# Performance work log

Measured on AMD Instinct MI355X. Metric: run time of the kernel, lower is better.

Reference implementation:

```python
import jax, jax.numpy as jnp
import numpy as np

G = 1.0      # gravitational constant from G_Nbody(graph, 1.0, eps=1e-10)
EPS = 1e-10  # softening epsilon
N_BODIES = 4096


def setup_inputs() -> dict:
    key = jax.random.key(0)
    kx, = jax.random.split(key, 1)
    x = jax.random.normal(kx, (N_BODIES, 4), dtype=jnp.float32)  # [N, 2q + 2p]
    m = jnp.ones((N_BODIES, 1), dtype=jnp.float32)               # node masses g.ndata['m']
    return {"x": x, "m": m}


def _hamiltonian(x, m):
    # x: [N, 4] = (q, p); m: [N, 1]
    q, p = jnp.split(x, 2, axis=-1)
    # Kinetic: faithful to create_kin's T[0,0,:].sum() -> all |p_j|^2 divided by 2*m_0
    K = jnp.sum(p * p) / (2.0 * m[0, 0])
    # Potential: all-pairs, Us[j, i] = G * m_i * m_j / (|q_j - q_i| + eps)
    diff = q[:, None, :] - q[None, :, :]          # [N, N, 2], diff[j, i] = q_j - q_i
    sq = jnp.sum(diff * diff, axis=-1)            # [N, N]
    n = x.shape[0]
    eye = jnp.eye(n, dtype=bool)
    dist = jnp.sqrt(jnp.where(eye, 1.0, sq))      # safe sqrt on diagonal (r=0 self-pair)
    mu = G * (m * m.T)                            # [N, N]
    # diagonal self-pair contributes constant mu/eps (zero q-gradient), as in original
    Us = jnp.where(eye, mu / EPS, mu / (dist + EPS))
    idx = jnp.arange(n)
    keep = idx[None, :] <= idx[:, None] + 1       # torch.tril(Us, diagonal=1)
    U = jnp.sum(jnp.where(keep, Us, 0.0))
    return K + U


def reference(x, m):
    # forward(t, x): dH/dx, then return cat(dH/dp, -dH/dq) (symplectic vector field)
    dHdx = jax.grad(_hamiltonian)(x, m)           # [N, 4]
    dHdq, dHdp = jnp.split(dHdx, 2, axis=-1)
    return jnp.concatenate((dHdp, -dHdq), axis=-1)
```

## Files before the change

### kernel.cpp

```cpp
#include <hip/hip_runtime.h>

#define NB 4096
#define TPB 1024
#define WPB (TPB / 64)
#define NBLK (NB / WPB)
#define NT (NB / 64)

__global__ __launch_bounds__(TPB) void nbody_wave(
    const float* __restrict__ x, const float* __restrict__ m,
    float4* __restrict__ out)
{
    __shared__ float2 q2[NB];
    __shared__ float  ms[NB];

    const int tid = threadIdx.x;

    #pragma unroll
    for (int t = 0; t < NB / TPB; ++t) {
        const int i = t * TPB + tid;
        const float4 xi = ((const float4*)x)[i];
        q2[i] = make_float2(xi.x, xi.y);
        ms[i] = m[i];
    }
    __syncthreads();

    const int wave = tid >> 6;
    const int lane = tid & 63;
    const int k = blockIdx.x * WPB + wave;

    const float2 qk = q2[k];
    const float qx = qk.x, qy = qk.y;
    float ax = 0.f, ay = 0.f;

    #pragma unroll 8
    for (int t = 0; t < NT; ++t) {
        const int i = t * 64 + lane;
        const float2 qi = q2[i];
        const float mi = ms[i];
        const float dx = qx - qi.x;
        const float dy = qy - qi.y;
        float sq = fmaf(dx, dx, dy * dy);
        sq = fmaxf(sq, 1e-12f);
        const float rinv = rsqrtf(sq);
        const float w = rinv * rinv * rinv * mi;
        ax = fmaf(dx, w, ax);
        ay = fmaf(dy, w, ay);
    }

    int nbi = -2;
    if (lane == 0) nbi = k - 1;
    else if (lane == 1) nbi = k + 1;
    if (nbi >= 0 && nbi < NB) {
        const float2 qi = q2[nbi];
        const float dx = qx - qi.x;
        const float dy = qy - qi.y;
        const float sq = fmaf(dx, dx, dy * dy);
        const float rinv = rsqrtf(sq);
        const float w = rinv * rinv * rinv * ms[nbi];
        ax = fmaf(dx, w, ax);
        ay = fmaf(dy, w, ay);
    }

    #pragma unroll
    for (int off = 32; off > 0; off >>= 1) {
        ax += __shfl_xor(ax, off);
        ay += __shfl_xor(ay, off);
    }

    if (lane == 0) {
        const float4 xk = ((const float4*)x)[k];
        const float mk = m[k];
        const float m0inv = 1.0f / m[0];
        out[k] = make_float4(xk.z * m0inv, xk.w * m0inv, ax * mk, ay * mk);
    }
}

extern "C" void kernel_launch(void* const* d_in, const int* in_sizes, int n_in,
                              void* d_out, int out_size, void* d_ws, size_t ws_size,
                              hipStream_t stream) {
    const float* x = (const float*)d_in[0];
    const float* m = (const float*)d_in[1];
    nbody_wave<<<dim3(NBLK), dim3(TPB), 0, stream>>>(x, m, (float4*)d_out);
}
```

Before: 12.40 us.

## Register-block four target bodies per wave and pack q,m into float4 LDS

```diff
diff --git a/kernel.cpp b/kernel.cpp
--- a/kernel.cpp
+++ b/kernel.cpp
@@ -1,77 +1,114 @@
 #include <hip/hip_runtime.h>
 
 #define NB 4096
-#define TPB 1024
-#define WPB (TPB / 64)
-#define NBLK (NB / WPB)
+#define TPB 256
+#define U 4
+#define NBLK (NB / (U * (TPB / 64)))
 #define NT (NB / 64)
 
-__global__ __launch_bounds__(TPB) void nbody_wave(
+__global__ __launch_bounds__(TPB) void nbody_u4(
     const float* __restrict__ x, const float* __restrict__ m,
     float4* __restrict__ out)
 {
-    __shared__ float2 q2[NB];
-    __shared__ float  ms[NB];
+    __shared__ float4 qm[NB];
 
     const int tid = threadIdx.x;
 
     #pragma unroll
     for (int t = 0; t < NB / TPB; ++t) {
-        const int i = t * TPB + tid;
-        const float4 xi = ((const float4*)x)[i];
-        q2[i] = make_float2(xi.x, xi.y);
-        ms[i] = m[i];
+        const int j = t * TPB + tid;
+        const float4 xj = ((const float4*)x)[j];
+        qm[j] = make_float4(xj.x, xj.y, m[j], 0.f);
     }
     __syncthreads();
 
-    const int wave = tid >> 6;
     const int lane = tid & 63;
-    const int k = blockIdx.x * WPB + wave;
+    const int W = blockIdx.x * (TPB / 64) + (tid >> 6);
+    const int kb = U * W;
 
-    const float2 qk = q2[k];
-    const float qx = qk.x, qy = qk.y;
-    float ax = 0.f, ay = 0.f;
+    const float4 xk0 = ((const float4*)x)[kb + 0];
+    const float4 xk1 = ((const float4*)x)[kb + 1];
+    const float4 xk2 = ((const float4*)x)[kb + 2];
+    const float4 xk3 = ((const float4*)x)[kb + 3];
+
+    float ax0 = 0.f, ay0 = 0.f, ax1 = 0.f, ay1 = 0.f;
+    float ax2 = 0.f, ay2 = 0.f, ax3 = 0.f, ay3 = 0.f;
 
     #pragma unroll 8
     for (int t = 0; t < NT; ++t) {
-        const int i = t * 64 + lane;
-        const float2 qi = q2[i];
-        const float mi = ms[i];
-        const float dx = qx - qi.x;
-        const float dy = qy - qi.y;
-        float sq = fmaf(dx, dx, dy * dy);
-        sq = fmaxf(sq, 1e-12f);
-        const float rinv = rsqrtf(sq);
-        const float w = rinv * rinv * rinv * mi;
-        ax = fmaf(dx, w, ax);
-        ay = fmaf(dy, w, ay);
+        const int j = t * 64 + lane;
+        const float4 s = qm[j];
+        {
+            const float dx = xk0.x - s.x, dy = xk0.y - s.y;
+            const float sq = fmaf(dx, dx, fmaf(dy, dy, 1e-20f));
+            const float r = __builtin_amdgcn_rsqf(sq);
+            const float w = r * r * r * s.z;
+            ax0 = fmaf(dx, w, ax0); ay0 = fmaf(dy, w, ay0);
+        }
+        {
+            const float dx = xk1.x - s.x, dy = xk1.y - s.y;
+            const float sq = fmaf(dx, dx, fmaf(dy, dy, 1e-20f));
+            const float r = __builtin_amdgcn_rsqf(sq);
+            const float w = r * r * r * s.z;
+            ax1 = fmaf(dx, w, ax1); ay1 = fmaf(dy, w, ay1);
+        }
+        {
+            const float dx = xk2.x - s.x, dy = xk2.y - s.y;
+            const float sq = fmaf(dx, dx, fmaf(dy, dy, 1e-20f));
+            const float r = __builtin_amdgcn_rsqf(sq);
+            const float w = r * r * r * s.z;
+            ax2 = fmaf(dx, w, ax2); ay2 = fmaf(dy, w, ay2);
+        }
+        {
+            const float dx = xk3.x - s.x, dy = xk3.y - s.y;
+            const float sq = fmaf(dx, dx, fmaf(dy, dy, 1e-20f));
+            const float r = __builtin_amdgcn_rsqf(sq);
+            const float w = r * r * r * s.z;
+            ax3 = fmaf(dx, w, ax3); ay3 = fmaf(dy, w, ay3);
+        }
     }
 
-    int nbi = -2;
-    if (lane == 0) nbi = k - 1;
-    else if (lane == 1) nbi = k + 1;
-    if (nbi >= 0 && nbi < NB) {
-        const float2 qi = q2[nbi];
-        const float dx = qx - qi.x;
-        const float dy = qy - qi.y;
-        const float sq = fmaf(dx, dx, dy * dy);
-        const float rinv = rsqrtf(sq);
-        const float w = rinv * rinv * rinv * ms[nbi];
-        ax = fmaf(dx, w, ax);
-        ay = fmaf(dy, w, ay);
+    {
+        const int body = lane >> 1;
+        const int k = kb + body;
+        const int nb = (lane & 1) ? k + 1 : k - 1;
+        float cx = 0.f, cy = 0.f;
+        if (lane < 8 && nb >= 0 && nb < NB) {
+            const float qx = (body == 0) ? xk0.x : (body == 1) ? xk1.x
+                           : (body == 2) ? xk2.x : xk3.x;
+            const float qy = (body == 0) ? xk0.y : (body == 1) ? xk1.y
+                           : (body == 2) ? xk2.y : xk3.y;
+            const float4 s = qm[nb];
+            const float dx = qx - s.x, dy = qy - s.y;
+            const float sq = fmaf(dx, dx, dy * dy);
+            const float r = __builtin_amdgcn_rsqf(sq);
+            const float w = r * r * r * s.z;
+            cx = dx * w; cy = dy * w;
+        }
+        ax0 += (body == 0) ? cx : 0.f;  ay0 += (body == 0) ? cy : 0.f;
+        ax1 += (body == 1) ? cx : 0.f;  ay1 += (body == 1) ? cy : 0.f;
+        ax2 += (body == 2) ? cx : 0.f;  ay2 += (body == 2) ? cy : 0.f;
+        ax3 += (body == 3) ? cx : 0.f;  ay3 += (body == 3) ? cy : 0.f;
     }
 
     #pragma unroll
     for (int off = 32; off > 0; off >>= 1) {
-        ax += __shfl_xor(ax, off);
-        ay += __shfl_xor(ay, off);
+        ax0 += __shfl_xor(ax0, off);  ay0 += __shfl_xor(ay0, off);
+        ax1 += __shfl_xor(ax1, off);  ay1 += __shfl_xor(ay1, off);
+        ax2 += __shfl_xor(ax2, off);  ay2 += __shfl_xor(ay2, off);
+        ax3 += __shfl_xor(ax3, off);  ay3 += __shfl_xor(ay3, off);
     }
 
-    if (lane == 0) {
-        const float4 xk = ((const float4*)x)[k];
-        const float mk = m[k];
+    if (lane < U) {
+        const int k = kb + lane;
+        const float4 xk = (lane == 0) ? xk0 : (lane == 1) ? xk1
+                        : (lane == 2) ? xk2 : xk3;
+        const float sx = (lane == 0) ? ax0 : (lane == 1) ? ax1
+                       : (lane == 2) ? ax2 : ax3;
+        const float sy = (lane == 0) ? ay0 : (lane == 1) ? ay1
+                       : (lane == 2) ? ay2 : ay3;
         const float m0inv = 1.0f / m[0];
-        out[k] = make_float4(xk.z * m0inv, xk.w * m0inv, ax * mk, ay * mk);
+        out[k] = make_float4(xk.z * m0inv, xk.w * m0inv, sx * m[k], sy * m[k]);
     }
 }
 
@@ -80,5 +117,5 @@
                               hipStream_t stream) {
     const float* x = (const float*)d_in[0];
     const float* m = (const float*)d_in[1];
-    nbody_wave<<<dim3(NBLK), dim3(TPB), 0, stream>>>(x, m, (float4*)d_out);
+    nbody_u4<<<dim3(NBLK), dim3(TPB), 0, stream>>>(x, m, (float4*)d_out);
 }
```

Result: no change. 12.46 us (+0.5%).
